# Performance work log

Measured on AMD Instinct MI355X. Metric: run time of the kernel, lower is better.

## Reference

```python
import jax, jax.numpy as jnp
import numpy as np

B, S, D, H = 4, 1024, 768, 12
E = D // H  # head dim = 64

def setup_inputs() -> dict:
    key = jax.random.key(0)
    ks = jax.random.split(key, 8)
    sd = 1.0 / np.sqrt(D)
    return {
        'x':    jax.random.normal(ks[0], (B, S, D), jnp.float32),
        'Wqkv': jax.random.normal(ks[1], (3 * D, D), jnp.float32) * sd,
        'Wl':   jax.random.normal(ks[2], (H, H), jnp.float32) * (1.0 / np.sqrt(H)),
        'bl':   jax.random.normal(ks[3], (H,), jnp.float32) * 0.01,
        'Ww':   jax.random.normal(ks[4], (H, H), jnp.float32) * (1.0 / np.sqrt(H)),
        'bw':   jax.random.normal(ks[5], (H,), jnp.float32) * 0.01,
        'Wp':   jax.random.normal(ks[6], (D, D), jnp.float32) * sd,
        'bp':   jax.random.normal(ks[7], (D,), jnp.float32) * 0.01,
    }

def reference(x, Wqkv, Wl, bl, Ww, bw, Wp, bp):
    # qkv: [B,S,3D] -> [B,S,3,H,E] -> q,k,v each [B,H,S,E]
    qkv = jnp.einsum('bsd,fd->bsf', x, Wqkv)
    qkv = qkv.reshape(B, S, 3, H, E).transpose(2, 0, 3, 1, 4)
    q, k, v = qkv[0], qkv[1], qkv[2]
    # NOTE: source computes but never applies the 1/sqrt(E) scale; stay faithful.
    attn = jnp.einsum('bhqe,bhke->bhqk', q, k)            # [B,H,S,S]
    # talking-heads mix before softmax: Linear over head axis
    attn = jnp.einsum('bhqk,gh->bgqk', attn, Wl) + bl[None, :, None, None]
    attn = jax.nn.softmax(attn, axis=-1)
    # talking-heads mix after softmax
    attn = jnp.einsum('bhqk,gh->bgqk', attn, Ww) + bw[None, :, None, None]
    out = jnp.einsum('bhqk,bhke->bhqe', attn, v)          # [B,H,S,E]
    out = out.transpose(0, 2, 1, 3).reshape(B, S, D)      # b h s e -> b s (h e)
    return jnp.einsum('bsd,fd->bsf', out, Wp) + bp
```

## Files before the change

### kernel.cpp

```cpp
#include <hip/hip_runtime.h>
#include <math.h>


typedef _Float16 f16;
typedef __attribute__((ext_vector_type(8))) _Float16 f16x8;
typedef __attribute__((ext_vector_type(2))) _Float16 f16x2;
typedef __attribute__((ext_vector_type(4))) float f32x4;
typedef __attribute__((ext_vector_type(2))) float f32x2;
typedef unsigned short u16;

__device__ __forceinline__ u16 f2h(float f) {
  f16 h = (f16)f;
  return __builtin_bit_cast(u16, h);
}
__device__ __forceinline__ unsigned pk2h(float a, float b) {
  return __builtin_bit_cast(unsigned, __builtin_amdgcn_cvt_pkrtz(a, b));
}

__device__ __forceinline__ void async16(const void* g, void* l) {
  __builtin_amdgcn_global_load_lds(
      (const __attribute__((address_space(1))) unsigned int*)g,
      (__attribute__((address_space(3))) unsigned int*)l, 16, 0, 0);
}

#define MFMA_F16(a, b, c) __builtin_amdgcn_mfma_f32_16x16x32_f16((a), (b), (c), 0, 0, 0)

__global__ __launch_bounds__(256) void k_prep(const float* __restrict__ x,
                                              const float* __restrict__ Wqkv,
                                              const float* __restrict__ Wp,
                                              u16* __restrict__ xh,
                                              u16* __restrict__ wh,
                                              u16* __restrict__ wph) {
  const int blk = blockIdx.x, t = threadIdx.x;
  if (blk < 3072) {
    int i = blk * 256 + t;
    float4 v = ((const float4*)x)[i];
    ((ushort4*)xh)[i] = make_ushort4(f2h(v.x), f2h(v.y), f2h(v.z), f2h(v.w));
  } else if (blk < 4800) {
    int i = (blk - 3072) * 256 + t;
    float4 v = ((const float4*)Wqkv)[i];
    ((ushort4*)wh)[i] = make_ushort4(f2h(v.x), f2h(v.y), f2h(v.z), f2h(v.w));
  } else {
    int i = (blk - 4800) * 256 + t;
    float4 v = ((const float4*)Wp)[i];
    ((ushort4*)wph)[i] = make_ushort4(f2h(v.x), f2h(v.y), f2h(v.z), f2h(v.w));
  }
}

__global__ __launch_bounds__(256) void k_qkv(const u16* __restrict__ Axh,
                                             const u16* __restrict__ Bwh,
                                             u16* __restrict__ qkf,
                                             u16* __restrict__ vbuf) {
  __shared__ u16 smem[16384];
  u16* As = smem;
  u16* Bs = smem + 4096;
  const int t = threadIdx.x, lane = t & 63, wave = t >> 6;
  const int wm = wave >> 1, wn = wave & 1;
  const int quad = lane >> 4, l16 = lane & 15;
  const int pid = blockIdx.x;
  const int group = pid / 144;
  const int rem = pid - group * 144;
  const int m0 = (group * 8 + (rem & 7)) * 128;
  const int n0 = (rem >> 3) * 128;
  const bool vblk = (n0 >= 1536);
  const int srow = t >> 2, sch = (t & 3) * 8;
  f32x4 acc[4][4];
#pragma unroll
  for (int i = 0; i < 4; ++i)
#pragma unroll
    for (int j = 0; j < 4; ++j) acc[i][j] = (f32x4){0.f, 0.f, 0.f, 0.f};
  for (int k0 = 0; k0 < 768; k0 += 32) {
    const size_t ga = (size_t)(m0 + srow) * 768 + k0 + sch;
    const size_t gb = (size_t)(n0 + srow) * 768 + k0 + sch;
    __syncthreads();
    async16(Axh + ga, &As[t * 8]);
    async16(Axh + ga + (size_t)64 * 768, &As[2048 + t * 8]);
    async16(Bwh + gb, &Bs[t * 8]);
    async16(Bwh + gb + (size_t)64 * 768, &Bs[2048 + t * 8]);
    __syncthreads();
    f16x8 af[4], bfr[4];
#pragma unroll
    for (int i = 0; i < 4; ++i) af[i] = *(const f16x8*)&As[(wm * 64 + i * 16 + l16) * 32 + quad * 8];
#pragma unroll
    for (int j = 0; j < 4; ++j) bfr[j] = *(const f16x8*)&Bs[(wn * 64 + j * 16 + l16) * 32 + quad * 8];
#pragma unroll
    for (int i = 0; i < 4; ++i)
#pragma unroll
      for (int j = 0; j < 4; ++j) acc[i][j] = MFMA_F16(af[i], bfr[j], acc[i][j]);
  }
  __syncthreads();
  u16* T = smem;
#pragma unroll
  for (int i = 0; i < 4; ++i)
#pragma unroll
    for (int j = 0; j < 4; ++j)
#pragma unroll
      for (int r = 0; r < 4; ++r) {
        const int row = wm * 64 + i * 16 + quad * 4 + r;
        const int col = wn * 64 + j * 16 + l16;
        T[row * 128 + (col ^ ((row & 7) << 4))] = f2h(acc[i][j][r]);
      }
  __syncthreads();
  const int row = t >> 1, halfc = (t & 1) * 64;
  const int sw = (row & 7) << 4;
  u16* dst = vblk ? (vbuf + (size_t)(m0 + row) * 768 + (n0 - 1536) + halfc)
                  : (qkf + (size_t)(m0 + row) * 1536 + n0 + halfc);
#pragma unroll
  for (int c = 0; c < 64; c += 8)
    *(uint4*)(dst + c) = *(const uint4*)&T[row * 128 + ((halfc + c) ^ sw)];
}

__global__ __launch_bounds__(256) void k_qk(const u16* __restrict__ qkf,
                                            u16* __restrict__ scbuf) {
  __shared__ u16 smem[4][4096];
  u16* As = smem[0]; u16* Bs = smem[1];
  const int t = threadIdx.x, lane = t & 63, wave = t >> 6;
  const int wm = wave >> 1, wn = wave & 1;
  const int quad = lane >> 4, l16 = lane & 15;
  const int bh = blockIdx.z, b = bh / 12, h = bh % 12;
  const int m0 = blockIdx.y * 128, n0 = blockIdx.x * 128;
  const int srow = t >> 2, sch = (t & 3) * 8;
  f32x4 acc[4][4];
#pragma unroll
  for (int i = 0; i < 4; ++i)
#pragma unroll
    for (int j = 0; j < 4; ++j) acc[i][j] = (f32x4){0.f, 0.f, 0.f, 0.f};
  for (int k0 = 0; k0 < 64; k0 += 32) {
    const size_t ga = (size_t)(b * 1024 + m0 + srow) * 1536 + h * 64 + k0 + sch;
    const size_t gb = (size_t)(b * 1024 + n0 + srow) * 1536 + 768 + h * 64 + k0 + sch;
    __syncthreads();
    async16(qkf + ga, &As[t * 8]);
    async16(qkf + ga + (size_t)64 * 1536, &As[2048 + t * 8]);
    async16(qkf + gb, &Bs[t * 8]);
    async16(qkf + gb + (size_t)64 * 1536, &Bs[2048 + t * 8]);
    __syncthreads();
    f16x8 af[4], bfr[4];
#pragma unroll
    for (int i = 0; i < 4; ++i) af[i] = *(const f16x8*)&As[(wm * 64 + i * 16 + l16) * 32 + quad * 8];
#pragma unroll
    for (int j = 0; j < 4; ++j) bfr[j] = *(const f16x8*)&Bs[(wn * 64 + j * 16 + l16) * 32 + quad * 8];
#pragma unroll
    for (int i = 0; i < 4; ++i)
#pragma unroll
      for (int j = 0; j < 4; ++j) acc[i][j] = MFMA_F16(af[i], bfr[j], acc[i][j]);
  }
  __syncthreads();
  u16* T = &smem[0][0];
#pragma unroll
  for (int i = 0; i < 4; ++i)
#pragma unroll
    for (int j = 0; j < 4; ++j)
#pragma unroll
      for (int r = 0; r < 4; ++r) {
        const int row = wm * 64 + i * 16 + quad * 4 + r;
        const int col = wn * 64 + j * 16 + l16;
        T[row * 128 + (col ^ ((row & 7) << 4))] = f2h(acc[i][j][r]);
      }
  __syncthreads();
  const int row = t >> 1, halfc = (t & 1) * 64;
  const int sw = (row & 7) << 4;
  u16* dst = scbuf + ((size_t)(b * 1024 + m0 + row) * 12 + h) * 1024 + n0 + halfc;
#pragma unroll
  for (int c = 0; c < 64; c += 8)
    *(uint4*)(dst + c) = *(const uint4*)&T[row * 128 + ((halfc + c) ^ sw)];
}

__global__ __launch_bounds__(256) void k_mix(u16* __restrict__ scbuf,
                                             const float* __restrict__ Wl,
                                             const float* __restrict__ bl,
                                             const float* __restrict__ Ww,
                                             const float* __restrict__ bw) {
  __shared__ float wl_s[144], ww_s[144], bl_s[12], bw_s[12];
  __shared__ float red[4][12];
  const int t = threadIdx.x, lane = t & 63, wave = t >> 6;
  const int bq = blockIdx.x, b = bq >> 10, q = bq & 1023;
  if (t < 144) { wl_s[t] = Wl[t]; ww_s[t] = Ww[t]; }
  if (t < 12)  { bl_s[t] = bl[t]; bw_s[t] = bw[t]; }
  const size_t rowbase = ((size_t)(b * 1024 + q) * 12) * 1024 + 4 * t;
  f32x2 raw[12][2];
#pragma unroll
  for (int h = 0; h < 12; ++h) {
    const u16* p = scbuf + rowbase + ((size_t)h << 10);
    uint2 u = *(const uint2*)p;
    f16x2 a01 = __builtin_bit_cast(f16x2, u.x);
    f16x2 a23 = __builtin_bit_cast(f16x2, u.y);
    raw[h][0] = (f32x2){(float)a01.x, (float)a01.y};
    raw[h][1] = (f32x2){(float)a23.x, (float)a23.y};
  }
  __syncthreads();
  f32x2 lg[12][2];
#pragma unroll
  for (int g = 0; g < 12; ++g) {
    f32x2 a0 = {bl_s[g] - 16.f, bl_s[g] - 16.f}, a1 = a0;
#pragma unroll
    for (int h = 0; h < 12; ++h) {
      const float wv = wl_s[g * 12 + h];
      const f32x2 w = {wv, wv};
      a0 = __builtin_elementwise_fma(w, raw[h][0], a0);
      a1 = __builtin_elementwise_fma(w, raw[h][1], a1);
    }
    lg[g][0] = a0; lg[g][1] = a1;
  }
  float sm[12];
#pragma unroll
  for (int g = 0; g < 12; ++g) {
    f32x2 e0, e1;
    e0.x = __expf(lg[g][0].x); e0.y = __expf(lg[g][0].y);
    e1.x = __expf(lg[g][1].x); e1.y = __expf(lg[g][1].y);
    lg[g][0] = e0; lg[g][1] = e1;
    f32x2 s2 = e0 + e1;
    sm[g] = s2.x + s2.y;
  }
#pragma unroll
  for (int off = 32; off > 0; off >>= 1)
#pragma unroll
    for (int g = 0; g < 12; ++g) sm[g] += __shfl_xor(sm[g], off);
  if (lane == 0) {
#pragma unroll
    for (int g = 0; g < 12; ++g) red[wave][g] = sm[g];
  }
  __syncthreads();
#pragma unroll
  for (int g = 0; g < 12; ++g) {
    const float inv = 1.0f / (red[0][g] + red[1][g] + red[2][g] + red[3][g]);
    const f32x2 iv = {inv, inv};
    lg[g][0] *= iv;
    lg[g][1] *= iv;
  }
#pragma unroll
  for (int g2 = 0; g2 < 12; ++g2) {
    f32x2 o0 = {bw_s[g2], bw_s[g2]}, o1 = o0;
#pragma unroll
    for (int h = 0; h < 12; ++h) {
      const float wv = ww_s[g2 * 12 + h];
      const f32x2 w = {wv, wv};
      o0 = __builtin_elementwise_fma(w, lg[h][0], o0);
      o1 = __builtin_elementwise_fma(w, lg[h][1], o1);
    }
    uint2 st = make_uint2(pk2h(o0.x, o0.y), pk2h(o1.x, o1.y));
    *(uint2*)(scbuf + rowbase + ((size_t)g2 << 10)) = st;
  }
}

__global__ __launch_bounds__(256) void k_pv(const u16* __restrict__ probs,
                                            const u16* __restrict__ vbuf,
                                            u16* __restrict__ ctx) {
  __shared__ u16 As[4096];
  __shared__ u16 Bs[64 * 40];
  const int t = threadIdx.x, lane = t & 63, wave = t >> 6;
  const int wm = wave >> 1, wn = wave & 1;
  const int quad = lane >> 4, l16 = lane & 15;
  const int bh = blockIdx.y, b = bh / 12, h = bh % 12;
  const int m0 = blockIdx.x * 128;
  const int srow = t >> 2, sch = (t & 3) * 8;
  const int ev = t & 63, s8 = (t >> 6) * 8;
  f32x4 acc[4][2];
#pragma unroll
  for (int i = 0; i < 4; ++i)
#pragma unroll
    for (int j = 0; j < 2; ++j) acc[i][j] = (f32x4){0.f, 0.f, 0.f, 0.f};
  for (int k0 = 0; k0 < 1024; k0 += 32) {
    const u16* vp = vbuf + (size_t)(b * 1024 + k0 + s8) * 768 + h * 64 + ev;
    u16 vcol[8];
#pragma unroll
    for (int i = 0; i < 8; ++i) vcol[i] = vp[(size_t)i * 768];
    __syncthreads();
    const u16* ga = probs + ((size_t)(b * 1024 + m0 + srow) * 12 + h) * 1024 + k0 + sch;
    async16(ga, &As[t * 8]);
    async16(ga + (size_t)64 * 12 * 1024, &As[2048 + t * 8]);
    *(ushort4*)&Bs[ev * 40 + s8] = make_ushort4(vcol[0], vcol[1], vcol[2], vcol[3]);
    *(ushort4*)&Bs[ev * 40 + s8 + 4] = make_ushort4(vcol[4], vcol[5], vcol[6], vcol[7]);
    __syncthreads();
    f16x8 af[4], bfr[2];
#pragma unroll
    for (int i = 0; i < 4; ++i) af[i] = *(const f16x8*)&As[(wm * 64 + i * 16 + l16) * 32 + quad * 8];
#pragma unroll
    for (int j = 0; j < 2; ++j) bfr[j] = *(const f16x8*)&Bs[(wn * 32 + j * 16 + l16) * 40 + quad * 8];
#pragma unroll
    for (int i = 0; i < 4; ++i)
#pragma unroll
      for (int j = 0; j < 2; ++j) acc[i][j] = MFMA_F16(af[i], bfr[j], acc[i][j]);
  }
#pragma unroll
  for (int i = 0; i < 4; ++i)
#pragma unroll
    for (int j = 0; j < 2; ++j)
#pragma unroll
      for (int r = 0; r < 4; ++r) {
        int q = m0 + wm * 64 + i * 16 + quad * 4 + r;
        int e = wn * 32 + j * 16 + l16;
        ctx[(size_t)(b * 1024 + q) * 768 + h * 64 + e] = f2h(acc[i][j][r]);
      }
}

__global__ __launch_bounds__(256) void k_oproj(const u16* __restrict__ A,
                                               const u16* __restrict__ Bm,
                                               const float* __restrict__ bp,
                                               float* __restrict__ out) {
  __shared__ u16 As[4096];
  __shared__ u16 Bs[4096];
  const int t = threadIdx.x, lane = t & 63, wave = t >> 6;
  const int wm = wave >> 1, wn = wave & 1;
  const int quad = lane >> 4, l16 = lane & 15;
  const int m0 = blockIdx.y * 128, n0 = blockIdx.x * 128;
  const int srow = t >> 2, sch = (t & 3) * 8;
  f32x4 acc[4][4];
#pragma unroll
  for (int i = 0; i < 4; ++i)
#pragma unroll
    for (int j = 0; j < 4; ++j) acc[i][j] = (f32x4){0.f, 0.f, 0.f, 0.f};
  for (int k0 = 0; k0 < 768; k0 += 32) {
    __syncthreads();
    const u16* ga = A + (size_t)(m0 + srow) * 768 + k0 + sch;
    const u16* gb = Bm + (size_t)(n0 + srow) * 768 + k0 + sch;
    async16(ga, &As[t * 8]);
    async16(ga + (size_t)64 * 768, &As[2048 + t * 8]);
    async16(gb, &Bs[t * 8]);
    async16(gb + (size_t)64 * 768, &Bs[2048 + t * 8]);
    __syncthreads();
    f16x8 af[4], bfr[4];
#pragma unroll
    for (int i = 0; i < 4; ++i) af[i] = *(const f16x8*)&As[(wm * 64 + i * 16 + l16) * 32 + quad * 8];
#pragma unroll
    for (int j = 0; j < 4; ++j) bfr[j] = *(const f16x8*)&Bs[(wn * 64 + j * 16 + l16) * 32 + quad * 8];
#pragma unroll
    for (int i = 0; i < 4; ++i)
#pragma unroll
      for (int j = 0; j < 4; ++j) acc[i][j] = MFMA_F16(af[i], bfr[j], acc[i][j]);
  }
#pragma unroll
  for (int i = 0; i < 4; ++i)
#pragma unroll
    for (int j = 0; j < 4; ++j)
#pragma unroll
      for (int r = 0; r < 4; ++r) {
        const int row = m0 + wm * 64 + i * 16 + quad * 4 + r;
        const int col = n0 + wn * 64 + j * 16 + l16;
        out[(size_t)row * 768 + col] = acc[i][j][r] + bp[col];
      }
}

extern "C" void kernel_launch(void* const* d_in, const int* in_sizes, int n_in,
                              void* d_out, int out_size, void* d_ws, size_t ws_size,
                              hipStream_t stream) {
  const float* x    = (const float*)d_in[0];
  const float* Wqkv = (const float*)d_in[1];
  const float* Wl   = (const float*)d_in[2];
  const float* bl   = (const float*)d_in[3];
  const float* Ww   = (const float*)d_in[4];
  const float* bw   = (const float*)d_in[5];
  const float* Wp   = (const float*)d_in[6];
  const float* bp   = (const float*)d_in[7];
  float* out = (float*)d_out;

  char* ws = (char*)d_ws;
  u16* scbuf = (u16*)(ws + 0);
  u16* qkf   = (u16*)(ws + 100663296ull);
  u16* vbuf  = (u16*)(ws + 113246208ull);
  u16* ctx   = (u16*)(ws + 119537664ull);
  u16* x_h   = (u16*)(ws + 125829120ull);
  u16* wq_h  = (u16*)(ws + 132120576ull);
  u16* wp_h  = (u16*)(ws + 135659520ull);

  hipLaunchKernelGGL(k_prep, dim3(5376), dim3(256), 0, stream,
                     x, Wqkv, Wp, x_h, wq_h, wp_h);
  hipLaunchKernelGGL(k_qkv,  dim3(576),      dim3(256), 0, stream, x_h, wq_h, qkf, vbuf);
  hipLaunchKernelGGL(k_qk,   dim3(8, 8, 48), dim3(256), 0, stream, qkf, scbuf);
  hipLaunchKernelGGL(k_mix,  dim3(4096),     dim3(256), 0, stream, scbuf, Wl, bl, Ww, bw);
  hipLaunchKernelGGL(k_pv,   dim3(8, 48),    dim3(256), 0, stream, scbuf, vbuf, ctx);
  hipLaunchKernelGGL(k_oproj, dim3(6, 32),   dim3(256), 0, stream, ctx, wp_h, bp, out);
}
```

Baseline: 246.4 us.

## Fuse QK^T with talking-heads mix via two-pass softmax recompute

Result: slower. 319.2 us (+29.6%).

```diff
diff --git a/kernel.cpp b/kernel.cpp
--- a/kernel.cpp
+++ b/kernel.cpp
@@ -110,135 +110,178 @@
     *(uint4*)(dst + c) = *(const uint4*)&T[row * 128 + ((halfc + c) ^ sw)];
 }
 
-__global__ __launch_bounds__(256) void k_qk(const u16* __restrict__ qkf,
-                                            u16* __restrict__ scbuf) {
-  __shared__ u16 smem[4][4096];
-  u16* As = smem[0]; u16* Bs = smem[1];
-  const int t = threadIdx.x, lane = t & 63, wave = t >> 6;
-  const int wm = wave >> 1, wn = wave & 1;
-  const int quad = lane >> 4, l16 = lane & 15;
-  const int bh = blockIdx.z, b = bh / 12, h = bh % 12;
-  const int m0 = blockIdx.y * 128, n0 = blockIdx.x * 128;
+__device__ __forceinline__ void qk_heads(const u16* __restrict__ qkf,
+                                         int b, int q0, int k0, int t,
+                                         u16* As, u16* Bs,
+                                         f32x4 (&acc)[12][2]) {
+  const int lane = t & 63, wave = t >> 6;
+  const int quad = lane >> 4, l16 = lane & 15;
+  (void)quad;
+#pragma unroll
+  for (int h = 0; h < 12; ++h)
+#pragma unroll
+    for (int j = 0; j < 2; ++j) acc[h][j] = (f32x4){0.f, 0.f, 0.f, 0.f};
   const int srow = t >> 2, sch = (t & 3) * 8;
-  f32x4 acc[4][4];
-#pragma unroll
-  for (int i = 0; i < 4; ++i)
-#pragma unroll
-    for (int j = 0; j < 4; ++j) acc[i][j] = (f32x4){0.f, 0.f, 0.f, 0.f};
-  for (int k0 = 0; k0 < 64; k0 += 32) {
-    const size_t ga = (size_t)(b * 1024 + m0 + srow) * 1536 + h * 64 + k0 + sch;
-    const size_t gb = (size_t)(b * 1024 + n0 + srow) * 1536 + 768 + h * 64 + k0 + sch;
-    __syncthreads();
-    async16(qkf + ga, &As[t * 8]);
-    async16(qkf + ga + (size_t)64 * 1536, &As[2048 + t * 8]);
-    async16(qkf + gb, &Bs[t * 8]);
-    async16(qkf + gb + (size_t)64 * 1536, &Bs[2048 + t * 8]);
-    __syncthreads();
-    f16x8 af[4], bfr[4];
-#pragma unroll
-    for (int i = 0; i < 4; ++i) af[i] = *(const f16x8*)&As[(wm * 64 + i * 16 + l16) * 32 + quad * 8];
-#pragma unroll
-    for (int j = 0; j < 4; ++j) bfr[j] = *(const f16x8*)&Bs[(wn * 64 + j * 16 + l16) * 32 + quad * 8];
-#pragma unroll
-    for (int i = 0; i < 4; ++i)
-#pragma unroll
-      for (int j = 0; j < 4; ++j) acc[i][j] = MFMA_F16(af[i], bfr[j], acc[i][j]);
+#pragma unroll
+  for (int h = 0; h < 12; ++h) {
+    __syncthreads();
+    {
+      const size_t ga = (size_t)(b * 1024 + q0 + srow) * 1536 + h * 64 + sch;
+      async16(qkf + ga, &As[t * 8]);
+      async16(qkf + ga + 32, &As[2048 + t * 8]);
+    }
+    if (t < 128) {
+      const size_t gb = (size_t)(b * 1024 + k0 + srow) * 1536 + 768 + h * 64 + sch;
+      async16(qkf + gb, &Bs[t * 8]);
+      async16(qkf + gb + 32, &Bs[1024 + t * 8]);
+    }
+    __syncthreads();
+#pragma unroll
+    for (int c = 0; c < 2; ++c) {
+      f16x8 af = *(const f16x8*)&As[c * 2048 + (wave * 16 + l16) * 32 + (lane >> 4) * 8];
+      f16x8 bf0 = *(const f16x8*)&Bs[c * 1024 + (l16) * 32 + (lane >> 4) * 8];
+      f16x8 bf1 = *(const f16x8*)&Bs[c * 1024 + (16 + l16) * 32 + (lane >> 4) * 8];
+      acc[h][0] = MFMA_F16(af, bf0, acc[h][0]);
+      acc[h][1] = MFMA_F16(af, bf1, acc[h][1]);
+    }
+  }
+}
+
+__device__ __forceinline__ void mix1_g(const f32x4 (&acc)[12][2], const float* wl_s,
+                                       float b0, int g, f32x4& L0, f32x4& L1) {
+  L0 = (f32x4){b0, b0, b0, b0};
+  L1 = L0;
+#pragma unroll
+  for (int h = 0; h < 12; ++h) {
+    const float w = wl_s[g * 12 + h];
+    const f32x4 wv = {w, w, w, w};
+    L0 = __builtin_elementwise_fma(wv, acc[h][0], L0);
+    L1 = __builtin_elementwise_fma(wv, acc[h][1], L1);
+  }
+}
+
+__global__ __launch_bounds__(256) void k_qkmix_sum(const u16* __restrict__ qkf,
+                                                   const float* __restrict__ Wl,
+                                                   const float* __restrict__ bl,
+                                                   float* __restrict__ dpart) {
+  __shared__ u16 As[4096];
+  __shared__ u16 Bs[2048];
+  __shared__ float wl_s[144], bl_s[12];
+  __shared__ float dred[768];
+  const int t = threadIdx.x;
+  if (t < 144) wl_s[t] = Wl[t];
+  if (t < 12) bl_s[t] = bl[t];
+  const int kt = blockIdx.x, qt = blockIdx.y, b = blockIdx.z;
+  const int q0 = qt * 64, k0 = kt * 32;
+  f32x4 acc[12][2];
+  qk_heads(qkf, b, q0, k0, t, As, Bs, acc);
+  const int lane = t & 63, wave = t >> 6;
+  const int quad = lane >> 4, l16 = lane & 15;
+  f32x4 rs[12];
+#pragma unroll
+  for (int g = 0; g < 12; ++g) {
+    f32x4 L0, L1;
+    mix1_g(acc, wl_s, bl_s[g] - 16.f, g, L0, L1);
+    f32x4 e0, e1;
+#pragma unroll
+    for (int r = 0; r < 4; ++r) { e0[r] = __expf(L0[r]); e1[r] = __expf(L1[r]); }
+    rs[g] = e0 + e1;
+  }
+#pragma unroll
+  for (int m = 1; m <= 8; m <<= 1) {
+#pragma unroll
+    for (int g = 0; g < 12; ++g) {
+      f32x4 o;
+#pragma unroll
+      for (int r = 0; r < 4; ++r) o[r] = __shfl_xor(rs[g][r], m);
+      rs[g] += o;
+    }
+  }
+  if (l16 == 0) {
+#pragma unroll
+    for (int g = 0; g < 12; ++g)
+#pragma unroll
+      for (int r = 0; r < 4; ++r)
+        dred[(wave * 16 + quad * 4 + r) * 12 + g] = rs[g][r];
   }
   __syncthreads();
-  u16* T = &smem[0][0];
-#pragma unroll
-  for (int i = 0; i < 4; ++i)
-#pragma unroll
-    for (int j = 0; j < 4; ++j)
-#pragma unroll
-      for (int r = 0; r < 4; ++r) {
-        const int row = wm * 64 + i * 16 + quad * 4 + r;
-        const int col = wn * 64 + j * 16 + l16;
-        T[row * 128 + (col ^ ((row & 7) << 4))] = f2h(acc[i][j][r]);
-      }
-  __syncthreads();
-  const int row = t >> 1, halfc = (t & 1) * 64;
-  const int sw = (row & 7) << 4;
-  u16* dst = scbuf + ((size_t)(b * 1024 + m0 + row) * 12 + h) * 1024 + n0 + halfc;
-#pragma unroll
-  for (int c = 0; c < 64; c += 8)
-    *(uint4*)(dst + c) = *(const uint4*)&T[row * 128 + ((halfc + c) ^ sw)];
-}
-
-__global__ __launch_bounds__(256) void k_mix(u16* __restrict__ scbuf,
-                                             const float* __restrict__ Wl,
-                                             const float* __restrict__ bl,
-                                             const float* __restrict__ Ww,
-                                             const float* __restrict__ bw) {
+  const size_t base = (size_t)((b * 16 + qt) * 32 + kt) * 768;
+  for (int s = t; s < 768; s += 256) dpart[base + s] = dred[s];
+}
+
+__global__ __launch_bounds__(256) void k_dsum(const float* __restrict__ dpart,
+                                              float* __restrict__ dfinal) {
+  const int blk = blockIdx.x;
+  const int bq = blk / 3, part = blk % 3;
+  const int slot = part * 256 + threadIdx.x;
+  const float* p = dpart + (size_t)bq * 24576 + slot;
+  float s = 0.f;
+#pragma unroll
+  for (int kt = 0; kt < 32; ++kt) s += p[kt * 768];
+  dfinal[(size_t)bq * 768 + slot] = 1.0f / s;
+}
+
+__global__ __launch_bounds__(256) void k_qkmix_store(const u16* __restrict__ qkf,
+                                                     const float* __restrict__ Wl,
+                                                     const float* __restrict__ bl,
+                                                     const float* __restrict__ Ww,
+                                                     const float* __restrict__ bw,
+                                                     const float* __restrict__ dfinal,
+                                                     u16* __restrict__ scbuf) {
+  __shared__ u16 As[4096];
+  __shared__ u16 Bs[2048];
+  __shared__ u16 Tout[64 * 40];
   __shared__ float wl_s[144], ww_s[144], bl_s[12], bw_s[12];
-  __shared__ float red[4][12];
-  const int t = threadIdx.x, lane = t & 63, wave = t >> 6;
-  const int bq = blockIdx.x, b = bq >> 10, q = bq & 1023;
+  __shared__ float dinv_s[768];
+  const int t = threadIdx.x;
   if (t < 144) { wl_s[t] = Wl[t]; ww_s[t] = Ww[t]; }
   if (t < 12)  { bl_s[t] = bl[t]; bw_s[t] = bw[t]; }
-  const size_t rowbase = ((size_t)(b * 1024 + q) * 12) * 1024 + 4 * t;
-  f32x2 raw[12][2];
-#pragma unroll
-  for (int h = 0; h < 12; ++h) {
-    const u16* p = scbuf + rowbase + ((size_t)h << 10);
-    uint2 u = *(const uint2*)p;
-    f16x2 a01 = __builtin_bit_cast(f16x2, u.x);
-    f16x2 a23 = __builtin_bit_cast(f16x2, u.y);
-    raw[h][0] = (f32x2){(float)a01.x, (float)a01.y};
-    raw[h][1] = (f32x2){(float)a23.x, (float)a23.y};
-  }
-  __syncthreads();
-  f32x2 lg[12][2];
+  const int kt = blockIdx.x, qt = blockIdx.y, b = blockIdx.z;
+  const int q0 = qt * 64, k0 = kt * 32;
+  {
+    const size_t dbase = (size_t)(b * 16 + qt) * 768;
+    for (int s = t; s < 768; s += 256) dinv_s[s] = dfinal[dbase + s];
+  }
+  f32x4 acc[12][2];
+  qk_heads(qkf, b, q0, k0, t, As, Bs, acc);
+  const int lane = t & 63, wave = t >> 6;
+  const int quad = lane >> 4, l16 = lane & 15;
+  f32x4 P[12][2];
 #pragma unroll
   for (int g = 0; g < 12; ++g) {
-    f32x2 a0 = {bl_s[g] - 16.f, bl_s[g] - 16.f}, a1 = a0;
+    f32x4 L0, L1;
+    mix1_g(acc, wl_s, bl_s[g] - 16.f, g, L0, L1);
+    f32x4 dv;
+#pragma unroll
+    for (int r = 0; r < 4; ++r) dv[r] = dinv_s[(wave * 16 + quad * 4 + r) * 12 + g];
+#pragma unroll
+    for (int r = 0; r < 4; ++r) {
+      P[g][0][r] = __expf(L0[r]) * dv[r];
+      P[g][1][r] = __expf(L1[r]) * dv[r];
+    }
+  }
+  const int orow = t >> 2, oc = (t & 3) * 8;
+  const size_t obase0 = (size_t)(b * 1024 + q0 + orow) * 12;
+#pragma unroll
+  for (int g2 = 0; g2 < 12; ++g2) {
+    f32x4 O0 = (f32x4){bw_s[g2], bw_s[g2], bw_s[g2], bw_s[g2]}, O1 = O0;
 #pragma unroll
     for (int h = 0; h < 12; ++h) {
-      const float wv = wl_s[g * 12 + h];
-      const f32x2 w = {wv, wv};
-      a0 = __builtin_elementwise_fma(w, raw[h][0], a0);
-      a1 = __builtin_elementwise_fma(w, raw[h][1], a1);
-    }
-    lg[g][0] = a0; lg[g][1] = a1;
-  }
-  float sm[12];
-#pragma unroll
-  for (int g = 0; g < 12; ++g) {
-    f32x2 e0, e1;
-    e0.x = __expf(lg[g][0].x); e0.y = __expf(lg[g][0].y);
-    e1.x = __expf(lg[g][1].x); e1.y = __expf(lg[g][1].y);
-    lg[g][0] = e0; lg[g][1] = e1;
-    f32x2 s2 = e0 + e1;
-    sm[g] = s2.x + s2.y;
-  }
-#pragma unroll
-  for (int off = 32; off > 0; off >>= 1)
-#pragma unroll
-    for (int g = 0; g < 12; ++g) sm[g] += __shfl_xor(sm[g], off);
-  if (lane == 0) {
-#pragma unroll
-    for (int g = 0; g < 12; ++g) red[wave][g] = sm[g];
-  }
-  __syncthreads();
-#pragma unroll
-  for (int g = 0; g < 12; ++g) {
-    const float inv = 1.0f / (red[0][g] + red[1][g] + red[2][g] + red[3][g]);
-    const f32x2 iv = {inv, inv};
-    lg[g][0] *= iv;
-    lg[g][1] *= iv;
-  }
-#pragma unroll
-  for (int g2 = 0; g2 < 12; ++g2) {
-    f32x2 o0 = {bw_s[g2], bw_s[g2]}, o1 = o0;
-#pragma unroll
-    for (int h = 0; h < 12; ++h) {
-      const float wv = ww_s[g2 * 12 + h];
-      const f32x2 w = {wv, wv};
-      o0 = __builtin_elementwise_fma(w, lg[h][0], o0);
-      o1 = __builtin_elementwise_fma(w, lg[h][1], o1);
-    }
-    uint2 st = make_uint2(pk2h(o0.x, o0.y), pk2h(o1.x, o1.y));
-    *(uint2*)(scbuf + rowbase + ((size_t)g2 << 10)) = st;
+      const float w = ww_s[g2 * 12 + h];
+      const f32x4 wv = {w, w, w, w};
+      O0 = __builtin_elementwise_fma(wv, P[h][0], O0);
+      O1 = __builtin_elementwise_fma(wv, P[h][1], O1);
+    }
+    __syncthreads();
+#pragma unroll
+    for (int r = 0; r < 4; ++r) {
+      const int row = wave * 16 + quad * 4 + r;
+      Tout[row * 40 + l16] = f2h(O0[r]);
+      Tout[row * 40 + 16 + l16] = f2h(O1[r]);
+    }
+    __syncthreads();
+    uint4 v = *(const uint4*)&Tout[orow * 40 + oc];
+    *(uint4*)(scbuf + (obase0 + g2) * 1024 + k0 + oc) = v;
   }
 }
 
@@ -354,19 +397,23 @@
   float* out = (float*)d_out;
 
   char* ws = (char*)d_ws;
-  u16* scbuf = (u16*)(ws + 0);
-  u16* qkf   = (u16*)(ws + 100663296ull);
-  u16* vbuf  = (u16*)(ws + 113246208ull);
-  u16* ctx   = (u16*)(ws + 119537664ull);
-  u16* x_h   = (u16*)(ws + 125829120ull);
-  u16* wq_h  = (u16*)(ws + 132120576ull);
-  u16* wp_h  = (u16*)(ws + 135659520ull);
+  u16* scbuf   = (u16*)(ws + 0);
+  u16* qkf     = (u16*)(ws + 100663296ull);
+  u16* vbuf    = (u16*)(ws + 113246208ull);
+  u16* ctx     = (u16*)(ws + 119537664ull);
+  float* dpart = (float*)(ws + 119537664ull);
+  u16* x_h     = (u16*)(ws + 125829120ull);
+  float* dfinal= (float*)(ws + 125829120ull);
+  u16* wq_h    = (u16*)(ws + 132120576ull);
+  u16* wp_h    = (u16*)(ws + 135659520ull);
 
   hipLaunchKernelGGL(k_prep, dim3(5376), dim3(256), 0, stream,
                      x, Wqkv, Wp, x_h, wq_h, wp_h);
-  hipLaunchKernelGGL(k_qkv,  dim3(576),      dim3(256), 0, stream, x_h, wq_h, qkf, vbuf);
-  hipLaunchKernelGGL(k_qk,   dim3(8, 8, 48), dim3(256), 0, stream, qkf, scbuf);
-  hipLaunchKernelGGL(k_mix,  dim3(4096),     dim3(256), 0, stream, scbuf, Wl, bl, Ww, bw);
-  hipLaunchKernelGGL(k_pv,   dim3(8, 48),    dim3(256), 0, stream, scbuf, vbuf, ctx);
-  hipLaunchKernelGGL(k_oproj, dim3(6, 32),   dim3(256), 0, stream, ctx, wp_h, bp, out);
-}
+  hipLaunchKernelGGL(k_qkv, dim3(576), dim3(256), 0, stream, x_h, wq_h, qkf, vbuf);
+  hipLaunchKernelGGL(k_qkmix_sum, dim3(32, 16, 4), dim3(256), 0, stream, qkf, Wl, bl, dpart);
+  hipLaunchKernelGGL(k_dsum, dim3(192), dim3(256), 0, stream, dpart, dfinal);
+  hipLaunchKernelGGL(k_qkmix_store, dim3(32, 16, 4), dim3(256), 0, stream,
+                     qkf, Wl, bl, Ww, bw, dfinal, scbuf);
+  hipLaunchKernelGGL(k_pv, dim3(8, 48), dim3(256), 0, stream, scbuf, vbuf, ctx);
+  hipLaunchKernelGGL(k_oproj, dim3(6, 32), dim3(256), 0, stream, ctx, wp_h, bp, out);
+}
```

## Use MFMA for talking-heads mixing and stage score rows in LDS

Applied to the files above, without the earlier changes.

Measured after the change: 247.6 us. Within noise of the previous version (+0.5%).

```diff
diff --git a/kernel.cpp b/kernel.cpp
--- a/kernel.cpp
+++ b/kernel.cpp
@@ -4,9 +4,11 @@
 
 typedef _Float16 f16;
 typedef __attribute__((ext_vector_type(8))) _Float16 f16x8;
+typedef __attribute__((ext_vector_type(4))) _Float16 f16x4;
 typedef __attribute__((ext_vector_type(2))) _Float16 f16x2;
 typedef __attribute__((ext_vector_type(4))) float f32x4;
 typedef __attribute__((ext_vector_type(2))) float f32x2;
+typedef __attribute__((ext_vector_type(2))) unsigned u32x2;
 typedef unsigned short u16;
 
 __device__ __forceinline__ u16 f2h(float f) {
@@ -24,6 +26,7 @@
 }
 
 #define MFMA_F16(a, b, c) __builtin_amdgcn_mfma_f32_16x16x32_f16((a), (b), (c), 0, 0, 0)
+#define MFMA16(a, b, c) __builtin_amdgcn_mfma_f32_16x16x16f16((a), (b), (c), 0, 0, 0)
 
 __global__ __launch_bounds__(256) void k_prep(const float* __restrict__ x,
                                               const float* __restrict__ Wqkv,
@@ -170,75 +173,85 @@
                                              const float* __restrict__ bl,
                                              const float* __restrict__ Ww,
                                              const float* __restrict__ bw) {
-  __shared__ float wl_s[144], ww_s[144], bl_s[12], bw_s[12];
-  __shared__ float red[4][12];
-  const int t = threadIdx.x, lane = t & 63, wave = t >> 6;
+  __shared__ u16 S[12 * 1032];
+  __shared__ float red[4][16];
+  const int t = threadIdx.x, lane = t & 63, wave = t >> 6;
+  const int quad = lane >> 4, l16 = lane & 15;
   const int bq = blockIdx.x, b = bq >> 10, q = bq & 1023;
-  if (t < 144) { wl_s[t] = Wl[t]; ww_s[t] = Ww[t]; }
-  if (t < 12)  { bl_s[t] = bl[t]; bw_s[t] = bw[t]; }
-  const size_t rowbase = ((size_t)(b * 1024 + q) * 12) * 1024 + 4 * t;
-  f32x2 raw[12][2];
-#pragma unroll
-  for (int h = 0; h < 12; ++h) {
-    const u16* p = scbuf + rowbase + ((size_t)h << 10);
-    uint2 u = *(const uint2*)p;
-    f16x2 a01 = __builtin_bit_cast(f16x2, u.x);
-    f16x2 a23 = __builtin_bit_cast(f16x2, u.y);
-    raw[h][0] = (f32x2){(float)a01.x, (float)a01.y};
-    raw[h][1] = (f32x2){(float)a23.x, (float)a23.y};
-  }
-  __syncthreads();
-  f32x2 lg[12][2];
-#pragma unroll
-  for (int g = 0; g < 12; ++g) {
-    f32x2 a0 = {bl_s[g] - 16.f, bl_s[g] - 16.f}, a1 = a0;
-#pragma unroll
-    for (int h = 0; h < 12; ++h) {
-      const float wv = wl_s[g * 12 + h];
-      const f32x2 w = {wv, wv};
-      a0 = __builtin_elementwise_fma(w, raw[h][0], a0);
-      a1 = __builtin_elementwise_fma(w, raw[h][1], a1);
+  const size_t qslab = (size_t)(b * 1024 + q) * 12288;
+#pragma unroll
+  for (int i = 0; i < 7; ++i) {
+    const int ci = i * 256 + t;
+    if (ci < 1548) {
+      const int row = ci / 129, c = ci - row * 129;
+      async16(scbuf + qslab + row * 1024 + c * 8, &S[ci * 8]);
     }
-    lg[g][0] = a0; lg[g][1] = a1;
-  }
-  float sm[12];
-#pragma unroll
-  for (int g = 0; g < 12; ++g) {
-    f32x2 e0, e1;
-    e0.x = __expf(lg[g][0].x); e0.y = __expf(lg[g][0].y);
-    e1.x = __expf(lg[g][1].x); e1.y = __expf(lg[g][1].y);
-    lg[g][0] = e0; lg[g][1] = e1;
-    f32x2 s2 = e0 + e1;
-    sm[g] = s2.x + s2.y;
-  }
-#pragma unroll
-  for (int off = 32; off > 0; off >>= 1)
-#pragma unroll
-    for (int g = 0; g < 12; ++g) sm[g] += __shfl_xor(sm[g], off);
-  if (lane == 0) {
-#pragma unroll
-    for (int g = 0; g < 12; ++g) red[wave][g] = sm[g];
-  }
-  __syncthreads();
-#pragma unroll
-  for (int g = 0; g < 12; ++g) {
-    const float inv = 1.0f / (red[0][g] + red[1][g] + red[2][g] + red[3][g]);
-    const f32x2 iv = {inv, inv};
-    lg[g][0] *= iv;
-    lg[g][1] *= iv;
-  }
-#pragma unroll
-  for (int g2 = 0; g2 < 12; ++g2) {
-    f32x2 o0 = {bw_s[g2], bw_s[g2]}, o1 = o0;
-#pragma unroll
-    for (int h = 0; h < 12; ++h) {
-      const float wv = ww_s[g2 * 12 + h];
-      const f32x2 w = {wv, wv};
-      o0 = __builtin_elementwise_fma(w, lg[h][0], o0);
-      o1 = __builtin_elementwise_fma(w, lg[h][1], o1);
+  }
+  const bool act = (quad < 3);
+  f16x4 Awl = (f16x4){0, 0, 0, 0}, Aww = (f16x4){0, 0, 0, 0};
+  if (act && l16 < 12) {
+    const float4 wl4 = *(const float4*)&Wl[l16 * 12 + quad * 4];
+    const float4 ww4 = *(const float4*)&Ww[l16 * 12 + quad * 4];
+    Awl[0] = (f16)wl4.x; Awl[1] = (f16)wl4.y; Awl[2] = (f16)wl4.z; Awl[3] = (f16)wl4.w;
+    Aww[0] = (f16)ww4.x; Aww[1] = (f16)ww4.y; Aww[2] = (f16)ww4.z; Aww[3] = (f16)ww4.w;
+  }
+  float blv[4], bwv[4];
+#pragma unroll
+  for (int r = 0; r < 4; ++r) {
+    blv[r] = act ? bl[quad * 4 + r] - 16.f : 0.f;
+    bwv[r] = act ? bw[quad * 4 + r] : 0.f;
+  }
+  int roff[4];
+#pragma unroll
+  for (int j = 0; j < 4; ++j) roff[j] = (quad * 4 + j) * 1032 + l16;
+  __syncthreads();
+  float Ev[16][4];
+  float a0 = 0.f, a1 = 0.f, a2 = 0.f, a3 = 0.f;
+#pragma unroll
+  for (int i = 0; i < 16; ++i) {
+    const int kb = (wave * 16 + i) * 16;
+    f16x4 B1 = (f16x4){0, 0, 0, 0};
+    if (act) {
+#pragma unroll
+      for (int j = 0; j < 4; ++j) B1[j] = __builtin_bit_cast(f16, S[roff[j] + kb]);
     }
-    uint2 st = make_uint2(pk2h(o0.x, o0.y), pk2h(o1.x, o1.y));
-    *(uint2*)(scbuf + rowbase + ((size_t)g2 << 10)) = st;
+    f32x4 c1 = (f32x4){blv[0], blv[1], blv[2], blv[3]};
+    c1 = MFMA16(Awl, B1, c1);
+    const float e0 = __expf(c1[0]), e1 = __expf(c1[1]);
+    const float e2 = __expf(c1[2]), e3 = __expf(c1[3]);
+    Ev[i][0] = e0; Ev[i][1] = e1; Ev[i][2] = e2; Ev[i][3] = e3;
+    a0 += e0; a1 += e1; a2 += e2; a3 += e3;
+  }
+#pragma unroll
+  for (int m = 1; m <= 8; m <<= 1) {
+    a0 += __shfl_xor(a0, m); a1 += __shfl_xor(a1, m);
+    a2 += __shfl_xor(a2, m); a3 += __shfl_xor(a3, m);
+  }
+  if (l16 == 0) {
+    red[wave][quad * 4 + 0] = a0; red[wave][quad * 4 + 1] = a1;
+    red[wave][quad * 4 + 2] = a2; red[wave][quad * 4 + 3] = a3;
+  }
+  __syncthreads();
+  float dinv[4];
+#pragma unroll
+  for (int r = 0; r < 4; ++r) {
+    const int g = quad * 4 + r;
+    dinv[r] = 1.0f / (red[0][g] + red[1][g] + red[2][g] + red[3][g]);
+  }
+  u16* const outp = scbuf + qslab + (size_t)quad * 4096 + l16;
+#pragma unroll
+  for (int i = 0; i < 16; ++i) {
+    const int kb = (wave * 16 + i) * 16;
+    const unsigned lo = pk2h(Ev[i][0] * dinv[0], Ev[i][1] * dinv[1]);
+    const unsigned hi = pk2h(Ev[i][2] * dinv[2], Ev[i][3] * dinv[3]);
+    u32x2 pw = {lo, hi};
+    const f16x4 Pf = __builtin_bit_cast(f16x4, pw);
+    f32x4 c2 = (f32x4){bwv[0], bwv[1], bwv[2], bwv[3]};
+    c2 = MFMA16(Aww, Pf, c2);
+    if (act) {
+#pragma unroll
+      for (int r = 0; r < 4; ++r) outp[r * 1024 + kb] = f2h(c2[r]);
+    }
   }
 }
 
```
